# Kernel optimization log

Hardware: AMD Instinct MI355X
Metric: run time of the kernel (lower is better)

Reference implementation:

```python
import jax, jax.numpy as jnp
import numpy as np

NEG = -10000.0
START_ID, END_ID, PAD_ID = 0, 1, 2
B, S, T = 512, 512, 128


def setup_inputs() -> dict:
    key = jax.random.key(0)
    k1, k2, k3, k4 = jax.random.split(key, 4)
    x = jax.random.normal(k1, (B, S, T), dtype=jnp.float32)
    tags = jax.random.randint(k2, (B, S), 0, T)
    # prefix-ones mask; lengths in [1, S-2] so the gather at mask.sum(1) is in-range
    lengths = jax.random.randint(k3, (B,), 1, S - 1)
    mask = (jnp.arange(S)[None, :] < lengths[:, None]).astype(jnp.float32)
    # torch xavier_normal_ on (T, T): std = sqrt(2 / (T + T))
    std = (2.0 / (T + T)) ** 0.5
    transition = std * jax.random.normal(k4, (T, T), dtype=jnp.float32)
    return {"x": x, "tags": tags, "mask": mask, "transition": transition}


def _crf_forward(x, mask, transition):
    # forward algorithm: log partition function, shape (B,)
    b, s, t = x.shape
    alpha0 = jnp.full((b, t), NEG, dtype=x.dtype).at[:, START_ID].set(0.0)

    def step(alpha, inp):
        x_t, m_t = inp  # (B,T), (B,)
        # scores[b, next, prev] = alpha[b, prev] + x_t[b, next] + transition[next, prev]
        scores = alpha[:, None, :] + x_t[:, :, None] + transition[None, :, :]
        new = jax.scipy.special.logsumexp(scores, axis=2)  # (B,T)
        m = m_t[:, None]
        return new * m + alpha * (1.0 - m), None

    alpha, _ = jax.lax.scan(step, alpha0, (jnp.swapaxes(x, 0, 1), jnp.swapaxes(mask, 0, 1)))
    return jax.scipy.special.logsumexp(alpha + transition[END_ID], axis=1)


def _crf_score(x, tags, mask, transition):
    # gold path score, shape (B,) — emission at t is paired with tags[:, t+1]
    b, s, t = x.shape
    em = jnp.take_along_axis(x[:, : s - 1], tags[:, 1:s, None], axis=2)[..., 0]  # (B,S-1)
    tr = transition[tags[:, 1:s], tags[:, : s - 1]]  # (B,S-1)
    score = jnp.sum((em + tr) * mask[:, : s - 1], axis=1)
    last_idx = mask.sum(axis=1).astype(jnp.int32)  # (B,)
    last_tag = jnp.take_along_axis(tags, last_idx[:, None], axis=1)[:, 0]
    return score + transition[END_ID, last_tag]


def reference(x, tags, mask, transition):
    fwd_score = _crf_forward(x, mask, transition)
    gold_score = _crf_score(x, tags, mask, transition)
    return jnp.mean(fwd_score - gold_score)
```

## Files before the change

kernel.cpp:

```cpp
#include <hip/hip_runtime.h>

#define NTAG 128
#define SEQ 512
#define NBATCH 512
#define END_ID 1

typedef _Float16 h2 __attribute__((ext_vector_type(2)));
typedef __fp16 fp16x2 __attribute__((ext_vector_type(2)));

#define LOG2E 1.4426950408889634f
#define LN2   0.6931471805599453f

__device__ __forceinline__ uint pack2(float a, float b) {
  fp16x2 h = __builtin_amdgcn_cvt_pkrtz(a, b);
  return __builtin_bit_cast(uint, h);
}
__device__ __forceinline__ h2 as_h2(uint u) { return __builtin_bit_cast(h2, u); }

__device__ __forceinline__ float fast_exp2(float x) {
#if __has_builtin(__builtin_amdgcn_exp2f)
  return __builtin_amdgcn_exp2f(x);
#else
  return exp2f(x);
#endif
}
__device__ __forceinline__ float fast_log2(float x) {
#if __has_builtin(__builtin_amdgcn_logf)
  return __builtin_amdgcn_logf(x);
#else
  return log2f(x);
#endif
}

#if __has_builtin(__builtin_amdgcn_fdot2)
#define FDOT2(pu, eu, acc) acc = __builtin_amdgcn_fdot2(as_h2(pu), as_h2(eu), acc, false)
#else
#define FDOT2(pu, eu, acc) do { h2 _p = as_h2(pu), _e = as_h2(eu); \
  acc = fmaf((float)_p.x, (float)_e.x, fmaf((float)_p.y, (float)_e.y, acc)); } while (0)
#endif

#define RL(v, l) ((uint)__builtin_amdgcn_readlane((int)(v), (l)))

__global__ __launch_bounds__(128) void crf_kernel(
    const float* __restrict__ x,
    const int*   __restrict__ tags,
    const float* __restrict__ mask,
    const float* __restrict__ trans,
    float* __restrict__ ws)
{
  const int b   = blockIdx.x;
  const int tid = threadIdx.x;
  const int w   = tid >> 6;
  const int l   = tid & 63;
  const int j   = (w << 6) + l;

  __shared__ float pbuf[2][NTAG];
  __shared__ float vbuf[NTAG];

  const float* xb   = x    + (size_t)b * SEQ * NTAG;
  const float* mrow = mask + (size_t)b * SEQ;
  const int*   trow = tags + (size_t)b * SEQ;

  float msum = 0.f;
  #pragma unroll
  for (int i = 0; i < SEQ / 64; ++i) msum += mrow[l + i * 64];
  #pragma unroll
  for (int off = 1; off < 64; off <<= 1) msum += __shfl_xor(msum, off);
  const int len = (int)msum;

  uint e[64];
  {
    const float4* tr = (const float4*)(trans + (size_t)j * NTAG);
    #pragma unroll
    for (int k4 = 0; k4 < 32; ++k4) {
      float4 t4 = tr[k4];
      e[2 * k4 + 0] = pack2(fast_exp2(t4.x * LOG2E), fast_exp2(t4.y * LOG2E));
      e[2 * k4 + 1] = pack2(fast_exp2(t4.z * LOG2E), fast_exp2(t4.w * LOG2E));
    }
  }

  float pcur = (j == 0) ? 1.f : 0.f;
  float M = 0.f;
  pbuf[0][j] = pcur;
  __syncthreads();

  const float* xj = xb + j;
  float xf0 = xj[0 * NTAG];
  float xf1 = xj[1 * NTAG];
  float xf2 = xj[2 * NTAG];
  float xf3 = xj[3 * NTAG];

#define CRF_STEP(XF, S_)                                                      \
  {                                                                           \
    const int g  = t + (S_);                                                  \
    const int rs = (S_) & 1;                        \
    const float exv = fast_exp2(XF * LOG2E);                  \
    XF = xj[(size_t)min(g + 4, len) * NTAG];         \
    const float2 pp = ((const float2*)pbuf[rs])[l];      \
    const float  p0 = pbuf[rs][0];                        \
    int c = ((__float_as_int(p0) >> 23) & 0xff) - 127;                        \
    c = c < -60 ? -60 : (c > 60 ? 60 : c);                                    \
    const float sc = __int_as_float((127 - c) << 23);             \
    const uint pk = pack2(fminf(pp.x * sc, 60000.f),                          \
                          fminf(pp.y * sc, 60000.f));                         \
    float q0 = 0.f, q1 = 0.f, q2 = 0.f, q3 = 0.f;                             \
    _Pragma("unroll")                                                         \
    for (int gg = 0; gg < 64; gg += 8) {                                      \
      const uint s0 = RL(pk, gg + 0), s1 = RL(pk, gg + 1);                    \
      const uint s2 = RL(pk, gg + 2), s3 = RL(pk, gg + 3);                    \
      const uint s4 = RL(pk, gg + 4), s5 = RL(pk, gg + 5);                    \
      const uint s6 = RL(pk, gg + 6), s7 = RL(pk, gg + 7);                    \
      FDOT2(s0, e[gg + 0], q0); FDOT2(s1, e[gg + 1], q1);                     \
      FDOT2(s2, e[gg + 2], q2); FDOT2(s3, e[gg + 3], q3);                     \
      FDOT2(s4, e[gg + 4], q0); FDOT2(s5, e[gg + 5], q1);                     \
      FDOT2(s6, e[gg + 6], q2); FDOT2(s7, e[gg + 7], q3);                     \
    }                                                                         \
    const float q  = (q0 + q1) + (q2 + q3);                                   \
    const float pn = q * exv;                                                 \
    const bool act = (g < len);                                               \
    pcur = act ? pn : pcur;                                                   \
    M    = act ? (M + (float)c) : M;                                          \
    pbuf[rs ^ 1][j] = pcur;                                                   \
    __syncthreads();                                                          \
  }

  for (int t = 0; t < len; t += 4) {
    CRF_STEP(xf0, 0)
    CRF_STEP(xf1, 1)
    CRF_STEP(xf2, 2)
    CRF_STEP(xf3, 3)
  }
#undef CRF_STEP

  const float a_ln = (M + fast_log2(pcur)) * LN2;
  vbuf[j] = a_ln;
  __syncthreads();

  if (w == 0) {
    const float2 te = ((const float2*)(trans + END_ID * NTAG))[l];
    const float v_lo = vbuf[2 * l]     + te.x;
    const float v_hi = vbuf[2 * l + 1] + te.y;
    float m2 = fmaxf(v_lo, v_hi);
    #pragma unroll
    for (int off = 1; off < 64; off <<= 1) m2 = fmaxf(m2, __shfl_xor(m2, off));
    float s = fast_exp2((v_lo - m2) * LOG2E) + fast_exp2((v_hi - m2) * LOG2E);
    #pragma unroll
    for (int off = 1; off < 64; off <<= 1) s += __shfl_xor(s, off);
    const float fwd = m2 + fast_log2(s) * LN2;

    float gacc = 0.f;
    for (int i = l; i < len; i += 64) {
      const int tn = trow[i + 1];
      const int tp = trow[i];
      gacc += xb[(size_t)i * NTAG + tn] + trans[tn * NTAG + tp];
    }
    #pragma unroll
    for (int off = 1; off < 64; off <<= 1) gacc += __shfl_xor(gacc, off);

    if (l == 0) {
      const float gold = gacc + trans[END_ID * NTAG + trow[len]];
      ws[b] = fwd - gold;
    }
  }
}

__global__ void reduce_kernel(const float* __restrict__ ws, float* __restrict__ out) {
  __shared__ float sm[8];
  const int tid = threadIdx.x;
  float v = ws[tid];
  #pragma unroll
  for (int off = 1; off < 64; off <<= 1) v += __shfl_xor(v, off);
  if ((tid & 63) == 0) sm[tid >> 6] = v;
  __syncthreads();
  if (tid == 0) {
    float s = 0.f;
    #pragma unroll
    for (int w = 0; w < 8; ++w) s += sm[w];
    out[0] = s * (1.0f / 512.0f);
  }
}

extern "C" void kernel_launch(void* const* d_in, const int* in_sizes, int n_in,
                              void* d_out, int out_size, void* d_ws, size_t ws_size,
                              hipStream_t stream) {
  const float* x     = (const float*)d_in[0];
  const int*   tags  = (const int*)d_in[1];
  const float* mask  = (const float*)d_in[2];
  const float* trans = (const float*)d_in[3];
  float*       ws    = (float*)d_ws;

  crf_kernel<<<NBATCH, 128, 0, stream>>>(x, tags, mask, trans, ws);
  reduce_kernel<<<1, 512, 0, stream>>>(ws, (float*)d_out);
}
```

Before: 465.6 us.

## Batch 16 sequences per wave and run the CRF recurrence on MFMA

Rewrites the forward recurrence so each 64-thread block handles 16 batch rows at once. The exp(transition) matrix is held in registers as f16 MFMA A-fragments, and the per-step matrix-vector products become 16x16x32 MFMA tiles, replacing per-lane readlane plus fdot2 and the shared-memory barriers of the old one-sequence-per-block design. Scaling now uses a shared exponent taken from the previous step's max across the wave instead of p0. This removes syncthreads and the serial dot-product latency, but launches only 32 blocks, so most CUs sit idle, and every wave runs to the longest length in its group. It also risks f16 overflow or underflow with the new scaling scheme.

```diff
diff --git a/kernel.cpp b/kernel.cpp
--- a/kernel.cpp
+++ b/kernel.cpp
@@ -4,8 +4,11 @@
 #define SEQ 512
 #define NBATCH 512
 #define END_ID 1
-
-typedef _Float16 h2 __attribute__((ext_vector_type(2)));
+#define GB 16
+#define EMARGIN 4
+
+typedef _Float16 v8h __attribute__((ext_vector_type(8)));
+typedef float f32x4 __attribute__((ext_vector_type(4)));
 typedef __fp16 fp16x2 __attribute__((ext_vector_type(2)));
 
 #define LOG2E 1.4426950408889634f
@@ -15,8 +18,6 @@
   fp16x2 h = __builtin_amdgcn_cvt_pkrtz(a, b);
   return __builtin_bit_cast(uint, h);
 }
-__device__ __forceinline__ h2 as_h2(uint u) { return __builtin_bit_cast(h2, u); }
-
 __device__ __forceinline__ float fast_exp2(float x) {
 #if __has_builtin(__builtin_amdgcn_exp2f)
   return __builtin_amdgcn_exp2f(x);
@@ -32,135 +33,167 @@
 #endif
 }
 
-#if __has_builtin(__builtin_amdgcn_fdot2)
-#define FDOT2(pu, eu, acc) acc = __builtin_amdgcn_fdot2(as_h2(pu), as_h2(eu), acc, false)
-#else
-#define FDOT2(pu, eu, acc) do { h2 _p = as_h2(pu), _e = as_h2(eu); \
-  acc = fmaf((float)_p.x, (float)_e.x, fmaf((float)_p.y, (float)_e.y, acc)); } while (0)
-#endif
-
-#define RL(v, l) ((uint)__builtin_amdgcn_readlane((int)(v), (l)))
-
-__global__ __launch_bounds__(128) void crf_kernel(
+__global__ __launch_bounds__(64, 1) void crf_kernel(
     const float* __restrict__ x,
     const int*   __restrict__ tags,
     const float* __restrict__ mask,
     const float* __restrict__ trans,
     float* __restrict__ ws)
 {
-  const int b   = blockIdx.x;
-  const int tid = threadIdx.x;
-  const int w   = tid >> 6;
-  const int l   = tid & 63;
-  const int j   = (w << 6) + l;
-
-  __shared__ float pbuf[2][NTAG];
-  __shared__ float vbuf[NTAG];
-
-  const float* xb   = x    + (size_t)b * SEQ * NTAG;
-  const float* mrow = mask + (size_t)b * SEQ;
-  const int*   trow = tags + (size_t)b * SEQ;
+  const int bg = blockIdx.x * GB;
+  const int l  = threadIdx.x;
+  const int m  = l & 15;
+  const int h  = l >> 4;
+
+  const int bb = bg + m;
+  const float* xb   = x    + (size_t)bb * SEQ * NTAG;
+  const int*   trow = tags + (size_t)bb * SEQ;
 
   float msum = 0.f;
-  #pragma unroll
-  for (int i = 0; i < SEQ / 64; ++i) msum += mrow[l + i * 64];
-  #pragma unroll
-  for (int off = 1; off < 64; off <<= 1) msum += __shfl_xor(msum, off);
+  {
+    const float4* m4 = (const float4*)(mask + (size_t)bb * SEQ);
+    #pragma unroll
+    for (int k = 0; k < 32; ++k) {
+      float4 v = m4[h * 32 + k];
+      msum += (v.x + v.y) + (v.z + v.w);
+    }
+    msum += __shfl_xor(msum, 16);
+    msum += __shfl_xor(msum, 32);
+  }
   const int len = (int)msum;
-
-  uint e[64];
-  {
-    const float4* tr = (const float4*)(trans + (size_t)j * NTAG);
-    #pragma unroll
-    for (int k4 = 0; k4 < 32; ++k4) {
-      float4 t4 = tr[k4];
-      e[2 * k4 + 0] = pack2(fast_exp2(t4.x * LOG2E), fast_exp2(t4.y * LOG2E));
-      e[2 * k4 + 1] = pack2(fast_exp2(t4.z * LOG2E), fast_exp2(t4.w * LOG2E));
+  int ml = len;
+  #pragma unroll
+  for (int off = 1; off < 64; off <<= 1) ml = max(ml, __shfl_xor(ml, off));
+  const int maxlenE = (ml + 1) & ~1;
+
+  v8h Afr[8][4];
+  #pragma unroll
+  for (int mt = 0; mt < 8; ++mt) {
+    const float* rowp = trans + (size_t)(mt * 16 + m) * NTAG;
+    #pragma unroll
+    for (int ks = 0; ks < 4; ++ks) {
+      float4 c0 = *(const float4*)(rowp + ks * 32 + h * 4);
+      float4 c1 = *(const float4*)(rowp + ks * 32 + 16 + h * 4);
+      v8h a;
+      a[0] = (_Float16)fast_exp2(c0.x * LOG2E);
+      a[1] = (_Float16)fast_exp2(c0.y * LOG2E);
+      a[2] = (_Float16)fast_exp2(c0.z * LOG2E);
+      a[3] = (_Float16)fast_exp2(c0.w * LOG2E);
+      a[4] = (_Float16)fast_exp2(c1.x * LOG2E);
+      a[5] = (_Float16)fast_exp2(c1.y * LOG2E);
+      a[6] = (_Float16)fast_exp2(c1.z * LOG2E);
+      a[7] = (_Float16)fast_exp2(c1.w * LOG2E);
+      Afr[mt][ks] = a;
     }
   }
 
-  float pcur = (j == 0) ? 1.f : 0.f;
+  v8h PkA[4], PkB[4];
+  #pragma unroll
+  for (int ks = 0; ks < 4; ++ks) {
+    v8h z;
+    #pragma unroll
+    for (int i = 0; i < 8; ++i) z[i] = (_Float16)0.0f;
+    PkA[ks] = z; PkB[ks] = z;
+  }
+  if (h == 0) PkA[0][0] = (_Float16)1.0f;
   float M = 0.f;
-  pbuf[0][j] = pcur;
-  __syncthreads();
-
-  const float* xj = xb + j;
-  float xf0 = xj[0 * NTAG];
-  float xf1 = xj[1 * NTAG];
-  float xf2 = xj[2 * NTAG];
-  float xf3 = xj[3 * NTAG];
-
-#define CRF_STEP(XF, S_)                                                      \
+  int eprev = 0;
+
+  const float4* xrow4 = (const float4*)xb;
+  float4 xA[8], xB[8];
+  #pragma unroll
+  for (int mt = 0; mt < 8; ++mt) xA[mt] = xrow4[mt * 4 + h];
+
+  const f32x4 zero4 = {0.f, 0.f, 0.f, 0.f};
+
+#define BODY(PS, PD, XC, XN, T_)                                              \
   {                                                                           \
-    const int g  = t + (S_);                                                  \
-    const int rs = (S_) & 1;                        \
-    const float exv = fast_exp2(XF * LOG2E);                  \
-    XF = xj[(size_t)min(g + 4, len) * NTAG];         \
-    const float2 pp = ((const float2*)pbuf[rs])[l];      \
-    const float  p0 = pbuf[rs][0];                        \
-    int c = ((__float_as_int(p0) >> 23) & 0xff) - 127;                        \
-    c = c < -60 ? -60 : (c > 60 ? 60 : c);                                    \
-    const float sc = __int_as_float((127 - c) << 23);             \
-    const uint pk = pack2(fminf(pp.x * sc, 60000.f),                          \
-                          fminf(pp.y * sc, 60000.f));                         \
-    float q0 = 0.f, q1 = 0.f, q2 = 0.f, q3 = 0.f;                             \
+    const int t_ = (T_);                                                      \
+    const bool act = (t_ < len);                                              \
     _Pragma("unroll")                                                         \
-    for (int gg = 0; gg < 64; gg += 8) {                                      \
-      const uint s0 = RL(pk, gg + 0), s1 = RL(pk, gg + 1);                    \
-      const uint s2 = RL(pk, gg + 2), s3 = RL(pk, gg + 3);                    \
-      const uint s4 = RL(pk, gg + 4), s5 = RL(pk, gg + 5);                    \
-      const uint s6 = RL(pk, gg + 6), s7 = RL(pk, gg + 7);                    \
-      FDOT2(s0, e[gg + 0], q0); FDOT2(s1, e[gg + 1], q1);                     \
-      FDOT2(s2, e[gg + 2], q2); FDOT2(s3, e[gg + 3], q3);                     \
-      FDOT2(s4, e[gg + 4], q0); FDOT2(s5, e[gg + 5], q1);                     \
-      FDOT2(s6, e[gg + 6], q2); FDOT2(s7, e[gg + 7], q3);                     \
+    for (int mt = 0; mt < 8; ++mt)                                            \
+      XN[mt] = xrow4[(size_t)(t_ + 1) * 32 + mt * 4 + h];                     \
+    const float csh = (float)(eprev + EMARGIN);                               \
+    float smax = 0.f;                                                         \
+    uint pu[8][2];                                                            \
+    _Pragma("unroll")                                                         \
+    for (int mt = 0; mt < 8; ++mt) {                                          \
+      f32x4 d = __builtin_amdgcn_mfma_f32_16x16x32_f16(Afr[mt][0], PS[0], zero4, 0, 0, 0); \
+      d = __builtin_amdgcn_mfma_f32_16x16x32_f16(Afr[mt][1], PS[1], d, 0, 0, 0); \
+      d = __builtin_amdgcn_mfma_f32_16x16x32_f16(Afr[mt][2], PS[2], d, 0, 0, 0); \
+      d = __builtin_amdgcn_mfma_f32_16x16x32_f16(Afr[mt][3], PS[3], d, 0, 0, 0); \
+      const float4 xv = XC[mt];                                               \
+      const float v0 = d[0] * fast_exp2(fmaf(xv.x, LOG2E, -csh));             \
+      const float v1 = d[1] * fast_exp2(fmaf(xv.y, LOG2E, -csh));             \
+      const float v2 = d[2] * fast_exp2(fmaf(xv.z, LOG2E, -csh));             \
+      const float v3 = d[3] * fast_exp2(fmaf(xv.w, LOG2E, -csh));             \
+      smax = fmaxf(smax, fmaxf(fmaxf(v0, v1), fmaxf(v2, v3)));                \
+      pu[mt][0] = pack2(v0, v1);                                              \
+      pu[mt][1] = pack2(v2, v3);                                              \
     }                                                                         \
-    const float q  = (q0 + q1) + (q2 + q3);                                   \
-    const float pn = q * exv;                                                 \
-    const bool act = (g < len);                                               \
-    pcur = act ? pn : pcur;                                                   \
-    M    = act ? (M + (float)c) : M;                                          \
-    pbuf[rs ^ 1][j] = pcur;                                                   \
-    __syncthreads();                                                          \
-  }
-
-  for (int t = 0; t < len; t += 4) {
-    CRF_STEP(xf0, 0)
-    CRF_STEP(xf1, 1)
-    CRF_STEP(xf2, 2)
-    CRF_STEP(xf3, 3)
-  }
-#undef CRF_STEP
-
-  const float a_ln = (M + fast_log2(pcur)) * LN2;
-  vbuf[j] = a_ln;
-  __syncthreads();
-
-  if (w == 0) {
-    const float2 te = ((const float2*)(trans + END_ID * NTAG))[l];
-    const float v_lo = vbuf[2 * l]     + te.x;
-    const float v_hi = vbuf[2 * l + 1] + te.y;
-    float m2 = fmaxf(v_lo, v_hi);
-    #pragma unroll
-    for (int off = 1; off < 64; off <<= 1) m2 = fmaxf(m2, __shfl_xor(m2, off));
-    float s = fast_exp2((v_lo - m2) * LOG2E) + fast_exp2((v_hi - m2) * LOG2E);
-    #pragma unroll
-    for (int off = 1; off < 64; off <<= 1) s += __shfl_xor(s, off);
-    const float fwd = m2 + fast_log2(s) * LN2;
-
-    float gacc = 0.f;
-    for (int i = l; i < len; i += 64) {
-      const int tn = trow[i + 1];
-      const int tp = trow[i];
-      gacc += xb[(size_t)i * NTAG + tn] + trans[tn * NTAG + tp];
+    _Pragma("unroll")                                                         \
+    for (int ks = 0; ks < 4; ++ks) {                                          \
+      uint4 q; q.x = pu[2 * ks][0]; q.y = pu[2 * ks][1];                      \
+      q.z = pu[2 * ks + 1][0]; q.w = pu[2 * ks + 1][1];                       \
+      const v8h nv = __builtin_bit_cast(v8h, q);                              \
+      PD[ks] = act ? nv : PS[ks];                                             \
+    }                                                                         \
+    smax = fmaxf(smax, __shfl_xor(smax, 16));                                 \
+    smax = fmaxf(smax, __shfl_xor(smax, 32));                                 \
+    int en = ((__float_as_int(smax) >> 23) & 255) - 127;                      \
+    en = en < -30 ? -30 : (en > 30 ? 30 : en);                                \
+    M     = act ? (M + csh) : M;                                              \
+    eprev = act ? en : eprev;                                                 \
+  }
+
+  for (int t = 0; t < maxlenE; t += 2) {
+    BODY(PkA, PkB, xA, xB, t)
+    BODY(PkB, PkA, xB, xA, t + 1)
+  }
+#undef BODY
+
+  const float* tE = trans + (size_t)END_ID * NTAG;
+  float vv[4][8];
+  float m2 = -3.4e38f;
+  #pragma unroll
+  for (int ks = 0; ks < 4; ++ks) {
+    float4 te0 = *(const float4*)(tE + ks * 32 + h * 4);
+    float4 te1 = *(const float4*)(tE + ks * 32 + 16 + h * 4);
+    #pragma unroll
+    for (int i = 0; i < 8; ++i) {
+      const float p  = (float)PkA[ks][i];
+      const float te = (i < 4)
+          ? ((i & 3) == 0 ? te0.x : (i & 3) == 1 ? te0.y : (i & 3) == 2 ? te0.z : te0.w)
+          : ((i & 3) == 0 ? te1.x : (i & 3) == 1 ? te1.y : (i & 3) == 2 ? te1.z : te1.w);
+      const float v = (M + fast_log2(p)) * LN2 + te;
+      vv[ks][i] = v;
+      m2 = fmaxf(m2, v);
     }
-    #pragma unroll
-    for (int off = 1; off < 64; off <<= 1) gacc += __shfl_xor(gacc, off);
-
-    if (l == 0) {
-      const float gold = gacc + trans[END_ID * NTAG + trow[len]];
-      ws[b] = fwd - gold;
-    }
+  }
+  m2 = fmaxf(m2, __shfl_xor(m2, 16));
+  m2 = fmaxf(m2, __shfl_xor(m2, 32));
+  float s = 0.f;
+  #pragma unroll
+  for (int ks = 0; ks < 4; ++ks)
+    #pragma unroll
+    for (int i = 0; i < 8; ++i)
+      s += fast_exp2((vv[ks][i] - m2) * LOG2E);
+  s += __shfl_xor(s, 16);
+  s += __shfl_xor(s, 32);
+  const float fwd = m2 + fast_log2(s) * LN2;
+
+  float g = 0.f;
+  for (int i = h; i < len; i += 4) {
+    const int tn = trow[i + 1];
+    const int tp = trow[i];
+    g += xb[(size_t)i * NTAG + tn] + trans[(size_t)tn * NTAG + tp];
+  }
+  g += __shfl_xor(g, 16);
+  g += __shfl_xor(g, 32);
+
+  if (h == 0) {
+    const float gold = g + trans[(size_t)END_ID * NTAG + trow[len]];
+    ws[bb] = fwd - gold;
   }
 }
 
@@ -189,6 +222,6 @@
   const float* trans = (const float*)d_in[3];
   float*       ws    = (float*)d_ws;
 
-  crf_kernel<<<NBATCH, 128, 0, stream>>>(x, tags, mask, trans, ws);
+  crf_kernel<<<NBATCH / GB, 64, 0, stream>>>(x, tags, mask, trans, ws);
   reduce_kernel<<<1, 512, 0, stream>>>(ws, (float*)d_out);
 }
```

Measured after the change: 543.7 us. 1.17x slower.
